# Performance work log

Measured on AMD Instinct MI355X. Metric: run time of the kernel, lower is better.

The kernel has to match this reference:

```python
import jax, jax.numpy as jnp
import numpy as np

N, K, D = 131072, 256, 128


def setup_inputs() -> dict:
    key = jax.random.key(0)
    k1, k2 = jax.random.split(key, 2)
    x = jax.random.normal(k1, (N, D), dtype=jnp.float32)
    mu = jax.random.normal(k2, (K, D), dtype=jnp.float32)
    prec = jnp.ones((D,), dtype=jnp.float32)
    return {"x": x, "mu": mu, "prec": prec}


def reference(x, mu, prec):
    # measure[n,k] = -0.5 * sum_d prec[d] * (x[n,d] - mu[k,d])**2
    # Expanded quadratic form avoids materializing the (N,K,D) diff tensor:
    #   sum_d prec*(x-mu)^2 = sum_d prec*x^2 - 2*sum_d (prec*x)*mu + sum_d prec*mu^2
    x_sq = jnp.einsum('nd,d->n', x * x, prec)            # (N,)
    mu_sq = jnp.einsum('kd,d->k', mu * mu, prec)         # (K,)
    cross = jnp.einsum('nd,d,kd->nk', x, prec, mu)       # (N,K)
    m = -0.5 * (x_sq[:, None] - 2.0 * cross + mu_sq[None, :])  # (N,K)
    return -jnp.sum(jax.nn.logsumexp(m, axis=1))
```

## Files before the change

kernel.cpp:

```cpp
#include <hip/hip_runtime.h>
#include <hip/hip_bf16.h>

#define N_ROWS 131072
#define K_MIX  256
#define D_DIM  128
#define LDSB_STRIDE 136

typedef float  f32x4  __attribute__((ext_vector_type(4)));
typedef short  bf16x8 __attribute__((ext_vector_type(8)));

#define LOG2E_F 1.44269504088896340736f
#define LN2_F   0.69314718055994530942f

#if __has_builtin(__builtin_amdgcn_exp2f)
#define EXP2F(x) __builtin_amdgcn_exp2f(x)
#else
#define EXP2F(x) exp2f(x)
#endif
#if __has_builtin(__builtin_amdgcn_logf)
#define LOG2F(x) __builtin_amdgcn_logf(x)
#else
#define LOG2F(x) __log2f(x)
#endif

__device__ inline bf16x8 pack8(float4 a, float4 b) {
    union { bf16x8 v; __hip_bfloat162 h[4]; } u;
    u.h[0] = __float22bfloat162_rn(make_float2(a.x, a.y));
    u.h[1] = __float22bfloat162_rn(make_float2(a.z, a.w));
    u.h[2] = __float22bfloat162_rn(make_float2(b.x, b.y));
    u.h[3] = __float22bfloat162_rn(make_float2(b.z, b.w));
    return u.v;
}

__global__ __launch_bounds__(256, 2)
void mixture_fused(const float* __restrict__ x,
                   const float* __restrict__ mu,
                   const float* __restrict__ prec,
                   float* __restrict__ out)
{
    __shared__ __align__(16) unsigned short sB[K_MIX * LDSB_STRIDE];
    __shared__ float sMusq[K_MIX];
    __shared__ float sPrec[D_DIM];
    __shared__ float sRed[4];

    const int tid  = threadIdx.x;
    const int lane = tid & 63;
    const int wave = tid >> 6;
    const int low4 = lane & 15;
    const int q    = lane >> 4;

    if (tid < 32) {
        float4 pv = ((const float4*)prec)[tid];
        pv.x *= LOG2E_F; pv.y *= LOG2E_F; pv.z *= LOG2E_F; pv.w *= LOG2E_F;
        *(float4*)&sPrec[tid * 4] = pv;
    }

    #pragma unroll 4
    for (int i = 0; i < 32; ++i) {
        const int idx = i * 256 + tid;
        const int row = idx >> 5;
        const int c4  = idx & 31;
        float4 mv = ((const float4*)mu)[idx];
        float4 pv = ((const float4*)prec)[c4];
        float px = mv.x * pv.x * LOG2E_F, py = mv.y * pv.y * LOG2E_F;
        float pz = mv.z * pv.z * LOG2E_F, pw = mv.w * pv.w * LOG2E_F;
        union { ushort4 u4; __hip_bfloat162 h[2]; } hh;
        hh.h[0] = __float22bfloat162_rn(make_float2(px, py));
        hh.h[1] = __float22bfloat162_rn(make_float2(pz, pw));
        *(ushort4*)&sB[row * LDSB_STRIDE + c4 * 4] = hh.u4;
        float ps = px * mv.x + py * mv.y + pz * mv.z + pw * mv.w;
        ps += __shfl_xor(ps, 1);  ps += __shfl_xor(ps, 2);
        ps += __shfl_xor(ps, 4);  ps += __shfl_xor(ps, 8);
        ps += __shfl_xor(ps, 16);
        if ((tid & 31) == 0) sMusq[row] = -0.5f * ps;
    }
    __syncthreads();

    const float4* x4 = (const float4*)x;
    const int rbase = blockIdx.x * 256 + wave * 32;
    const float4* xr0 = x4 + (size_t)(rbase + low4) * 32;
    const float4* xr1 = x4 + (size_t)(rbase + low4 + 16) * 32;

    float lacc = 0.f;

    #pragma unroll 1
    for (int rg = 0; rg < 2; ++rg) {
        const float4* p0 = xr0 + rg * 128 * 32;
        const float4* p1 = xr1 + rg * 128 * 32;

        float4 xv[4][4];
        #pragma unroll
        for (int k = 0; k < 4; ++k) {
            const int d4 = k * 8 + q * 2;
            xv[k][0] = p0[d4]; xv[k][1] = p0[d4 + 1];
            xv[k][2] = p1[d4]; xv[k][3] = p1[d4 + 1];
        }

        float xsA = 0.f, xsB = 0.f;
        bf16x8 a0[4], a1[4];
        #pragma unroll
        for (int k = 0; k < 4; ++k) {
            const int d4 = k * 8 + q * 2;
            float4 pa = *(const float4*)&sPrec[d4 * 4];
            float4 pb = *(const float4*)&sPrec[d4 * 4 + 4];
            xsA += pa.x*xv[k][0].x*xv[k][0].x + pa.y*xv[k][0].y*xv[k][0].y
                 + pa.z*xv[k][0].z*xv[k][0].z + pa.w*xv[k][0].w*xv[k][0].w;
            xsB += pb.x*xv[k][1].x*xv[k][1].x + pb.y*xv[k][1].y*xv[k][1].y
                 + pb.z*xv[k][1].z*xv[k][1].z + pb.w*xv[k][1].w*xv[k][1].w;
            xsA += pa.x*xv[k][2].x*xv[k][2].x + pa.y*xv[k][2].y*xv[k][2].y
                 + pa.z*xv[k][2].z*xv[k][2].z + pa.w*xv[k][2].w*xv[k][2].w;
            xsB += pb.x*xv[k][3].x*xv[k][3].x + pb.y*xv[k][3].y*xv[k][3].y
                 + pb.z*xv[k][3].z*xv[k][3].z + pb.w*xv[k][3].w*xv[k][3].w;
            a0[k] = pack8(xv[k][0], xv[k][1]);
            a1[k] = pack8(xv[k][2], xv[k][3]);
        }

        float m_run[2][4], s_run[2][4];
        #pragma unroll
        for (int m = 0; m < 2; ++m)
            #pragma unroll
            for (int i = 0; i < 4; ++i) { m_run[m][i] = -3.0e38f; s_run[m][i] = 0.f; }

        #pragma unroll 1
        for (int h = 0; h < 2; ++h) {
            f32x4 acc[2][8];
            #pragma unroll
            for (int c = 0; c < 8; ++c) {
                float mneg = sMusq[(h * 8 + c) * 16 + low4];
                #pragma unroll
                for (int i = 0; i < 4; ++i) { acc[0][c][i] = mneg; acc[1][c][i] = mneg; }
            }

            #pragma unroll
            for (int k = 0; k < 4; ++k) {
                #pragma unroll
                for (int c = 0; c < 8; ++c) {
                    const unsigned short* bp =
                        &sB[((h * 8 + c) * 16 + low4) * LDSB_STRIDE + k * 32 + q * 8];
                    bf16x8 b = *(const bf16x8*)bp;
                    acc[0][c] = __builtin_amdgcn_mfma_f32_16x16x32_bf16(a0[k], b, acc[0][c], 0, 0, 0);
                    acc[1][c] = __builtin_amdgcn_mfma_f32_16x16x32_bf16(a1[k], b, acc[1][c], 0, 0, 0);
                }
            }

            #pragma unroll
            for (int m = 0; m < 2; ++m) {
                #pragma unroll
                for (int i = 0; i < 4; ++i) {
                    float v0 = acc[m][0][i], v1 = acc[m][1][i];
                    float v2 = acc[m][2][i], v3 = acc[m][3][i];
                    float v4 = acc[m][4][i], v5 = acc[m][5][i];
                    float v6 = acc[m][6][i], v7 = acc[m][7][i];
                    float hmax = fmaxf(fmaxf(fmaxf(v0, v1), fmaxf(v2, v3)),
                                       fmaxf(fmaxf(v4, v5), fmaxf(v6, v7)));
                    float hsum = EXP2F(v0 - hmax) + EXP2F(v1 - hmax)
                               + EXP2F(v2 - hmax) + EXP2F(v3 - hmax)
                               + EXP2F(v4 - hmax) + EXP2F(v5 - hmax)
                               + EXP2F(v6 - hmax) + EXP2F(v7 - hmax);
                    float mr = m_run[m][i];
                    float mn = fmaxf(mr, hmax);
                    s_run[m][i] = s_run[m][i] * EXP2F(mr - mn) + hsum * EXP2F(hmax - mn);
                    m_run[m][i] = mn;
                }
            }
        }

        #pragma unroll
        for (int m = 0; m < 2; ++m) {
            #pragma unroll
            for (int i = 0; i < 4; ++i) {
                float mr = m_run[m][i], sr = s_run[m][i];
                #pragma unroll
                for (int step = 1; step <= 8; step <<= 1) {
                    float mo = __shfl_xor(mr, step);
                    float so = __shfl_xor(sr, step);
                    float mn = fmaxf(mr, mo);
                    sr = sr * EXP2F(mr - mn) + so * EXP2F(mo - mn);
                    mr = mn;
                }
                if (low4 == 0) lacc -= mr + LOG2F(sr);
            }
        }
        lacc += 0.5f * (xsA + xsB);
    }

    lacc *= LN2_F;

    lacc += __shfl_xor(lacc, 32); lacc += __shfl_xor(lacc, 16);
    lacc += __shfl_xor(lacc, 8);  lacc += __shfl_xor(lacc, 4);
    lacc += __shfl_xor(lacc, 2);  lacc += __shfl_xor(lacc, 1);
    if (lane == 0) sRed[wave] = lacc;
    __syncthreads();
    if (tid == 0) atomicAdd(out, sRed[0] + sRed[1] + sRed[2] + sRed[3]);
}

extern "C" void kernel_launch(void* const* d_in, const int* in_sizes, int n_in,
                              void* d_out, int out_size, void* d_ws, size_t ws_size,
                              hipStream_t stream) {
    const float* x    = (const float*)d_in[0];
    const float* mu   = (const float*)d_in[1];
    const float* prec = (const float*)d_in[2];
    float* out = (float*)d_out;

    hipMemsetAsync(d_out, 0, sizeof(float), stream);
    mixture_fused<<<N_ROWS / 256, 256, 0, stream>>>(x, mu, prec, out);
}
```

Measured before the change: 119.6 us.

## Halve rows per block and stream mu in two LDS halves

Each block now processes 128 rows instead of 256 and stages the mixture centers into LDS in two halves of 128, so the LDS footprint is halved. The aim is higher occupancy and more blocks to hide latency, and the x loads are issued before mu staging so they can overlap. In exchange, every block redoes the mu scaling and bf16 conversion for twice as many blocks overall, and an extra barrier separates the two halves.

```diff
diff --git a/kernel.cpp b/kernel.cpp
--- a/kernel.cpp
+++ b/kernel.cpp
@@ -4,7 +4,9 @@
 #define N_ROWS 131072
 #define K_MIX  256
 #define D_DIM  128
+#define KHALF  128
 #define LDSB_STRIDE 136
+#define ROWS_PER_BLOCK 128
 
 typedef float  f32x4  __attribute__((ext_vector_type(4)));
 typedef short  bf16x8 __attribute__((ext_vector_type(8)));
@@ -38,9 +40,8 @@
                    const float* __restrict__ prec,
                    float* __restrict__ out)
 {
-    __shared__ __align__(16) unsigned short sB[K_MIX * LDSB_STRIDE];
-    __shared__ float sMusq[K_MIX];
-    __shared__ float sPrec[D_DIM];
+    __shared__ __align__(16) unsigned short sB[KHALF * LDSB_STRIDE];
+    __shared__ float sMusq[KHALF];
     __shared__ float sRed[4];
 
     const int tid  = threadIdx.x;
@@ -49,60 +50,31 @@
     const int low4 = lane & 15;
     const int q    = lane >> 4;
 
-    if (tid < 32) {
-        float4 pv = ((const float4*)prec)[tid];
-        pv.x *= LOG2E_F; pv.y *= LOG2E_F; pv.z *= LOG2E_F; pv.w *= LOG2E_F;
-        *(float4*)&sPrec[tid * 4] = pv;
-    }
-
-    #pragma unroll 4
-    for (int i = 0; i < 32; ++i) {
-        const int idx = i * 256 + tid;
-        const int row = idx >> 5;
-        const int c4  = idx & 31;
-        float4 mv = ((const float4*)mu)[idx];
-        float4 pv = ((const float4*)prec)[c4];
-        float px = mv.x * pv.x * LOG2E_F, py = mv.y * pv.y * LOG2E_F;
-        float pz = mv.z * pv.z * LOG2E_F, pw = mv.w * pv.w * LOG2E_F;
-        union { ushort4 u4; __hip_bfloat162 h[2]; } hh;
-        hh.h[0] = __float22bfloat162_rn(make_float2(px, py));
-        hh.h[1] = __float22bfloat162_rn(make_float2(pz, pw));
-        *(ushort4*)&sB[row * LDSB_STRIDE + c4 * 4] = hh.u4;
-        float ps = px * mv.x + py * mv.y + pz * mv.z + pw * mv.w;
-        ps += __shfl_xor(ps, 1);  ps += __shfl_xor(ps, 2);
-        ps += __shfl_xor(ps, 4);  ps += __shfl_xor(ps, 8);
-        ps += __shfl_xor(ps, 16);
-        if ((tid & 31) == 0) sMusq[row] = -0.5f * ps;
-    }
-    __syncthreads();
-
     const float4* x4 = (const float4*)x;
-    const int rbase = blockIdx.x * 256 + wave * 32;
+    const float4* p4 = (const float4*)prec;
+    const int rbase = blockIdx.x * ROWS_PER_BLOCK + wave * 32;
     const float4* xr0 = x4 + (size_t)(rbase + low4) * 32;
     const float4* xr1 = x4 + (size_t)(rbase + low4 + 16) * 32;
 
-    float lacc = 0.f;
-
-    #pragma unroll 1
-    for (int rg = 0; rg < 2; ++rg) {
-        const float4* p0 = xr0 + rg * 128 * 32;
-        const float4* p1 = xr1 + rg * 128 * 32;
-
-        float4 xv[4][4];
+    float4 xv[4][4];
+    #pragma unroll
+    for (int k = 0; k < 4; ++k) {
+        const int d4 = k * 8 + q * 2;
+        xv[k][0] = xr0[d4]; xv[k][1] = xr0[d4 + 1];
+        xv[k][2] = xr1[d4]; xv[k][3] = xr1[d4 + 1];
+    }
+
+    float xs;
+    bf16x8 a0[4], a1[4];
+    {
+        float xsA = 0.f, xsB = 0.f;
         #pragma unroll
         for (int k = 0; k < 4; ++k) {
             const int d4 = k * 8 + q * 2;
-            xv[k][0] = p0[d4]; xv[k][1] = p0[d4 + 1];
-            xv[k][2] = p1[d4]; xv[k][3] = p1[d4 + 1];
-        }
-
-        float xsA = 0.f, xsB = 0.f;
-        bf16x8 a0[4], a1[4];
-        #pragma unroll
-        for (int k = 0; k < 4; ++k) {
-            const int d4 = k * 8 + q * 2;
-            float4 pa = *(const float4*)&sPrec[d4 * 4];
-            float4 pb = *(const float4*)&sPrec[d4 * 4 + 4];
+            float4 pa = p4[d4];
+            float4 pb = p4[d4 + 1];
+            pa.x *= LOG2E_F; pa.y *= LOG2E_F; pa.z *= LOG2E_F; pa.w *= LOG2E_F;
+            pb.x *= LOG2E_F; pb.y *= LOG2E_F; pb.z *= LOG2E_F; pb.w *= LOG2E_F;
             xsA += pa.x*xv[k][0].x*xv[k][0].x + pa.y*xv[k][0].y*xv[k][0].y
                  + pa.z*xv[k][0].z*xv[k][0].z + pa.w*xv[k][0].w*xv[k][0].w;
             xsB += pb.x*xv[k][1].x*xv[k][1].x + pb.y*xv[k][1].y*xv[k][1].y
@@ -114,76 +86,101 @@
             a0[k] = pack8(xv[k][0], xv[k][1]);
             a1[k] = pack8(xv[k][2], xv[k][3]);
         }
-
-        float m_run[2][4], s_run[2][4];
-        #pragma unroll
-        for (int m = 0; m < 2; ++m)
-            #pragma unroll
-            for (int i = 0; i < 4; ++i) { m_run[m][i] = -3.0e38f; s_run[m][i] = 0.f; }
-
-        #pragma unroll 1
-        for (int h = 0; h < 2; ++h) {
-            f32x4 acc[2][8];
+        xs = xsA + xsB;
+    }
+
+    float m_run[2][4], s_run[2][4];
+    #pragma unroll
+    for (int m = 0; m < 2; ++m)
+        #pragma unroll
+        for (int i = 0; i < 4; ++i) { m_run[m][i] = -3.0e38f; s_run[m][i] = 0.f; }
+
+    float lacc = 0.f;
+
+    #pragma unroll 1
+    for (int e = 0; e < 2; ++e) {
+        if (e) __syncthreads();
+
+        #pragma unroll 4
+        for (int i = 0; i < 16; ++i) {
+            const int idx = i * 256 + tid;
+            const int row = idx >> 5;
+            const int c4  = idx & 31;
+            float4 mv = ((const float4*)mu)[e * 4096 + idx];
+            float4 pv = p4[c4];
+            float px = mv.x * pv.x * LOG2E_F, py = mv.y * pv.y * LOG2E_F;
+            float pz = mv.z * pv.z * LOG2E_F, pw = mv.w * pv.w * LOG2E_F;
+            union { ushort4 u4; __hip_bfloat162 h[2]; } hh;
+            hh.h[0] = __float22bfloat162_rn(make_float2(px, py));
+            hh.h[1] = __float22bfloat162_rn(make_float2(pz, pw));
+            *(ushort4*)&sB[row * LDSB_STRIDE + c4 * 4] = hh.u4;
+            float ps = px * mv.x + py * mv.y + pz * mv.z + pw * mv.w;
+            ps += __shfl_xor(ps, 1);  ps += __shfl_xor(ps, 2);
+            ps += __shfl_xor(ps, 4);  ps += __shfl_xor(ps, 8);
+            ps += __shfl_xor(ps, 16);
+            if ((tid & 31) == 0) sMusq[row] = -0.5f * ps;
+        }
+        __syncthreads();
+
+        f32x4 acc[2][8];
+        #pragma unroll
+        for (int c = 0; c < 8; ++c) {
+            float mneg = sMusq[c * 16 + low4];
+            #pragma unroll
+            for (int i = 0; i < 4; ++i) { acc[0][c][i] = mneg; acc[1][c][i] = mneg; }
+        }
+
+        #pragma unroll
+        for (int k = 0; k < 4; ++k) {
             #pragma unroll
             for (int c = 0; c < 8; ++c) {
-                float mneg = sMusq[(h * 8 + c) * 16 + low4];
-                #pragma unroll
-                for (int i = 0; i < 4; ++i) { acc[0][c][i] = mneg; acc[1][c][i] = mneg; }
+                const unsigned short* bp =
+                    &sB[(c * 16 + low4) * LDSB_STRIDE + k * 32 + q * 8];
+                bf16x8 b = *(const bf16x8*)bp;
+                acc[0][c] = __builtin_amdgcn_mfma_f32_16x16x32_bf16(a0[k], b, acc[0][c], 0, 0, 0);
+                acc[1][c] = __builtin_amdgcn_mfma_f32_16x16x32_bf16(a1[k], b, acc[1][c], 0, 0, 0);
             }
-
-            #pragma unroll
-            for (int k = 0; k < 4; ++k) {
-                #pragma unroll
-                for (int c = 0; c < 8; ++c) {
-                    const unsigned short* bp =
-                        &sB[((h * 8 + c) * 16 + low4) * LDSB_STRIDE + k * 32 + q * 8];
-                    bf16x8 b = *(const bf16x8*)bp;
-                    acc[0][c] = __builtin_amdgcn_mfma_f32_16x16x32_bf16(a0[k], b, acc[0][c], 0, 0, 0);
-                    acc[1][c] = __builtin_amdgcn_mfma_f32_16x16x32_bf16(a1[k], b, acc[1][c], 0, 0, 0);
-                }
+        }
+
+        #pragma unroll
+        for (int m = 0; m < 2; ++m) {
+            #pragma unroll
+            for (int i = 0; i < 4; ++i) {
+                float v0 = acc[m][0][i], v1 = acc[m][1][i];
+                float v2 = acc[m][2][i], v3 = acc[m][3][i];
+                float v4 = acc[m][4][i], v5 = acc[m][5][i];
+                float v6 = acc[m][6][i], v7 = acc[m][7][i];
+                float hmax = fmaxf(fmaxf(fmaxf(v0, v1), fmaxf(v2, v3)),
+                                   fmaxf(fmaxf(v4, v5), fmaxf(v6, v7)));
+                float hsum = EXP2F(v0 - hmax) + EXP2F(v1 - hmax)
+                           + EXP2F(v2 - hmax) + EXP2F(v3 - hmax)
+                           + EXP2F(v4 - hmax) + EXP2F(v5 - hmax)
+                           + EXP2F(v6 - hmax) + EXP2F(v7 - hmax);
+                float mr = m_run[m][i];
+                float mn = fmaxf(mr, hmax);
+                s_run[m][i] = s_run[m][i] * EXP2F(mr - mn) + hsum * EXP2F(hmax - mn);
+                m_run[m][i] = mn;
             }
-
-            #pragma unroll
-            for (int m = 0; m < 2; ++m) {
-                #pragma unroll
-                for (int i = 0; i < 4; ++i) {
-                    float v0 = acc[m][0][i], v1 = acc[m][1][i];
-                    float v2 = acc[m][2][i], v3 = acc[m][3][i];
-                    float v4 = acc[m][4][i], v5 = acc[m][5][i];
-                    float v6 = acc[m][6][i], v7 = acc[m][7][i];
-                    float hmax = fmaxf(fmaxf(fmaxf(v0, v1), fmaxf(v2, v3)),
-                                       fmaxf(fmaxf(v4, v5), fmaxf(v6, v7)));
-                    float hsum = EXP2F(v0 - hmax) + EXP2F(v1 - hmax)
-                               + EXP2F(v2 - hmax) + EXP2F(v3 - hmax)
-                               + EXP2F(v4 - hmax) + EXP2F(v5 - hmax)
-                               + EXP2F(v6 - hmax) + EXP2F(v7 - hmax);
-                    float mr = m_run[m][i];
-                    float mn = fmaxf(mr, hmax);
-                    s_run[m][i] = s_run[m][i] * EXP2F(mr - mn) + hsum * EXP2F(hmax - mn);
-                    m_run[m][i] = mn;
-                }
+        }
+    }
+
+    #pragma unroll
+    for (int m = 0; m < 2; ++m) {
+        #pragma unroll
+        for (int i = 0; i < 4; ++i) {
+            float mr = m_run[m][i], sr = s_run[m][i];
+            #pragma unroll
+            for (int step = 1; step <= 8; step <<= 1) {
+                float mo = __shfl_xor(mr, step);
+                float so = __shfl_xor(sr, step);
+                float mn = fmaxf(mr, mo);
+                sr = sr * EXP2F(mr - mn) + so * EXP2F(mo - mn);
+                mr = mn;
             }
-        }
-
-        #pragma unroll
-        for (int m = 0; m < 2; ++m) {
-            #pragma unroll
-            for (int i = 0; i < 4; ++i) {
-                float mr = m_run[m][i], sr = s_run[m][i];
-                #pragma unroll
-                for (int step = 1; step <= 8; step <<= 1) {
-                    float mo = __shfl_xor(mr, step);
-                    float so = __shfl_xor(sr, step);
-                    float mn = fmaxf(mr, mo);
-                    sr = sr * EXP2F(mr - mn) + so * EXP2F(mo - mn);
-                    mr = mn;
-                }
-                if (low4 == 0) lacc -= mr + LOG2F(sr);
-            }
-        }
-        lacc += 0.5f * (xsA + xsB);
-    }
-
+            if (low4 == 0) lacc -= mr + LOG2F(sr);
+        }
+    }
+    lacc += 0.5f * xs;
     lacc *= LN2_F;
 
     lacc += __shfl_xor(lacc, 32); lacc += __shfl_xor(lacc, 16);
@@ -203,5 +200,5 @@
     float* out = (float*)d_out;
 
     hipMemsetAsync(d_out, 0, sizeof(float), stream);
-    mixture_fused<<<N_ROWS / 256, 256, 0, stream>>>(x, mu, prec, out);
+    mixture_fused<<<N_ROWS / ROWS_PER_BLOCK, 256, 0, stream>>>(x, mu, prec, out);
 }
```

Result: slower. 141.7 us (+18.4%).

## Precompute bf16 mu table once and stream it into LDS via global_load_lds

Applied to the files above, without the earlier changes.

Moves the per-block conversion of mu into scaled bf16 and the mu-squared norms into a separate prep kernel that writes a padded table to workspace. The main kernel then fills LDS with direct global-to-LDS DMA loads instead of each of 512 blocks redoing the conversion and shuffles. This adds an extra launch and a dependency on the workspace, and relies on global_load_lds, whose per-wave LDS addressing must match the padded layout.

```diff
diff --git a/kernel.cpp b/kernel.cpp
--- a/kernel.cpp
+++ b/kernel.cpp
@@ -5,6 +5,7 @@
 #define K_MIX  256
 #define D_DIM  128
 #define LDSB_STRIDE 136
+#define B_CHUNKS (K_MIX * LDSB_STRIDE / 8)
 
 typedef float  f32x4  __attribute__((ext_vector_type(4)));
 typedef short  bf16x8 __attribute__((ext_vector_type(8)));
@@ -32,11 +33,39 @@
     return u.v;
 }
 
+__global__ void prep_kernel(const float* __restrict__ mu,
+                            const float* __restrict__ prec,
+                            unsigned short* __restrict__ Bp,
+                            float* __restrict__ musq)
+{
+    int idx = blockIdx.x * 256 + threadIdx.x;
+    int row = idx >> 5;
+    int c4  = idx & 31;
+    float4 mv = ((const float4*)mu)[idx];
+    float4 pv = ((const float4*)prec)[c4];
+    float px = mv.x * pv.x * LOG2E_F, py = mv.y * pv.y * LOG2E_F;
+    float pz = mv.z * pv.z * LOG2E_F, pw = mv.w * pv.w * LOG2E_F;
+    union { ushort4 u4; __hip_bfloat162 h[2]; } h;
+    h.h[0] = __float22bfloat162_rn(make_float2(px, py));
+    h.h[1] = __float22bfloat162_rn(make_float2(pz, pw));
+    *(ushort4*)&Bp[row * LDSB_STRIDE + c4 * 4] = h.u4;
+    if (c4 == 31) {
+        bf16x8 z = (bf16x8)0;
+        *(bf16x8*)&Bp[row * LDSB_STRIDE + 128] = z;
+    }
+    float ps = px * mv.x + py * mv.y + pz * mv.z + pw * mv.w;
+    ps += __shfl_xor(ps, 1);  ps += __shfl_xor(ps, 2);
+    ps += __shfl_xor(ps, 4);  ps += __shfl_xor(ps, 8);
+    ps += __shfl_xor(ps, 16);
+    if ((threadIdx.x & 31) == 0) musq[row] = -0.5f * ps;
+}
+
 __global__ __launch_bounds__(256, 2)
-void mixture_fused(const float* __restrict__ x,
-                   const float* __restrict__ mu,
-                   const float* __restrict__ prec,
-                   float* __restrict__ out)
+void mixture_main(const float* __restrict__ x,
+                  const unsigned short* __restrict__ Bp,
+                  const float* __restrict__ musqg,
+                  const float* __restrict__ prec,
+                  float* __restrict__ out)
 {
     __shared__ __align__(16) unsigned short sB[K_MIX * LDSB_STRIDE];
     __shared__ float sMusq[K_MIX];
@@ -49,30 +78,23 @@
     const int low4 = lane & 15;
     const int q    = lane >> 4;
 
-    if (tid < 32) {
-        float4 pv = ((const float4*)prec)[tid];
-        pv.x *= LOG2E_F; pv.y *= LOG2E_F; pv.z *= LOG2E_F; pv.w *= LOG2E_F;
-        *(float4*)&sPrec[tid * 4] = pv;
-    }
-
-    #pragma unroll 4
-    for (int i = 0; i < 32; ++i) {
-        const int idx = i * 256 + tid;
-        const int row = idx >> 5;
-        const int c4  = idx & 31;
-        float4 mv = ((const float4*)mu)[idx];
-        float4 pv = ((const float4*)prec)[c4];
-        float px = mv.x * pv.x * LOG2E_F, py = mv.y * pv.y * LOG2E_F;
-        float pz = mv.z * pv.z * LOG2E_F, pw = mv.w * pv.w * LOG2E_F;
-        union { ushort4 u4; __hip_bfloat162 h[2]; } hh;
-        hh.h[0] = __float22bfloat162_rn(make_float2(px, py));
-        hh.h[1] = __float22bfloat162_rn(make_float2(pz, pw));
-        *(ushort4*)&sB[row * LDSB_STRIDE + c4 * 4] = hh.u4;
-        float ps = px * mv.x + py * mv.y + pz * mv.z + pw * mv.w;
-        ps += __shfl_xor(ps, 1);  ps += __shfl_xor(ps, 2);
-        ps += __shfl_xor(ps, 4);  ps += __shfl_xor(ps, 8);
-        ps += __shfl_xor(ps, 16);
-        if ((tid & 31) == 0) sMusq[row] = -0.5f * ps;
+    {
+        #pragma unroll
+        for (int i = 0; i < B_CHUNKS / 256; ++i) {
+            const int chunk = i * 256 + wave * 64;
+            __builtin_amdgcn_global_load_lds(
+                (const __attribute__((address_space(1))) unsigned int*)
+                    &Bp[(size_t)(chunk + lane) * 8],
+                (__attribute__((address_space(3))) unsigned int*)
+                    &sB[(size_t)chunk * 8],
+                16, 0, 0);
+        }
+        sMusq[tid] = musqg[tid];
+        if (tid < 32) {
+            float4 pv = ((const float4*)prec)[tid];
+            pv.x *= LOG2E_F; pv.y *= LOG2E_F; pv.z *= LOG2E_F; pv.w *= LOG2E_F;
+            *(float4*)&sPrec[tid * 4] = pv;
+        }
     }
     __syncthreads();
 
@@ -202,6 +224,10 @@
     const float* prec = (const float*)d_in[2];
     float* out = (float*)d_out;
 
+    unsigned short* Bp = (unsigned short*)d_ws;
+    float* musq = (float*)((char*)d_ws + K_MIX * LDSB_STRIDE * 2);
+
     hipMemsetAsync(d_out, 0, sizeof(float), stream);
-    mixture_fused<<<N_ROWS / 256, 256, 0, stream>>>(x, mu, prec, out);
-}
+    prep_kernel<<<32, 256, 0, stream>>>(mu, prec, Bp, musq);
+    mixture_main<<<N_ROWS / 256, 256, 0, stream>>>(x, Bp, musq, prec, out);
+}
```

After: 109.8 us. 1.09x faster.
